# Performance work log

Measured on AMD Instinct MI355X. Metric: run time of the kernel, lower is better.

The kernel has to match this reference:

```python
import jax, jax.numpy as jnp
import numpy as np

N_NODES = 50000
N_EDGES = 800000
FEATS = 128
HIDDEN = 64
CLASSES = 64


def graph_conv(x, edges):
    """GCN-style symmetric-normalized aggregation over an edge list (no self-loops;
    self information is supplied via the concat in the host module)."""
    src, dst = edges[0], edges[1]
    ones = jnp.ones((edges.shape[1],), dtype=x.dtype)
    deg = jax.ops.segment_sum(ones, dst, num_segments=N_NODES)
    inv_sqrt = jax.lax.rsqrt(jnp.maximum(deg, 1.0))
    coef = inv_sqrt[src] * inv_sqrt[dst]            # [E]
    msg = x[src] * coef[:, None]                     # [E, H] gather
    return jax.ops.segment_sum(msg, dst, num_segments=N_NODES)  # [N, H] scatter


def setup_inputs() -> dict:
    key = jax.random.key(0)
    ks = jax.random.split(key, 16)
    def lin(k, out_d, in_d):
        return jax.random.normal(k, (out_d, in_d), dtype=jnp.float32) / np.sqrt(in_d)
    x = jax.random.normal(ks[0], (N_NODES, FEATS), dtype=jnp.float32)
    edges = jax.random.randint(ks[1], (2, N_EDGES), 0, N_NODES, dtype=jnp.int64)
    return {
        "x": x,
        "edges": edges,
        "W1": lin(ks[2], HIDDEN, FEATS),
        "b1": jnp.zeros((HIDDEN,), dtype=jnp.float32),
        "W2": lin(ks[3], HIDDEN, 2 * HIDDEN),
        "A2a": lin(ks[4], HIDDEN, HIDDEN),
        "A2b": lin(ks[5], HIDDEN, HIDDEN),
        "W3": lin(ks[6], HIDDEN, 2 * HIDDEN),
        "A3a": lin(ks[7], HIDDEN, HIDDEN),
        "A3b": lin(ks[8], HIDDEN, HIDDEN),
        "W4": lin(ks[9], CLASSES, 2 * HIDDEN),
        "A4a": lin(ks[10], CLASSES, HIDDEN),
        "A4b": lin(ks[11], CLASSES, HIDDEN),
    }


def _block(x, edges, W, Aa, Ab):
    # relu(Linear(cat[x, conv(x)]) + att_a(x) * att_b(x))
    h = graph_conv(x, edges)
    cat = jnp.concatenate([x, h], axis=1)            # [N, 2H]
    return jax.nn.relu(cat @ W.T + (x @ Aa.T) * (x @ Ab.T))


def reference(x, edges, W1, b1, W2, A2a, A2b, W3, A3a, A3b, W4, A4a, A4b):
    x = jax.nn.relu(x @ W1.T + b1)                   # [N, H]
    x = _block(x, edges, W2, A2a, A2b)               # [N, H]
    x = _block(x, edges, W3, A3a, A3b)               # [N, H]
    x = _block(x, edges, W4, A4a, A4b)               # [N, C]
    return x
```

## Files before the change

### kernel.cpp

```cpp
#include <hip/hip_runtime.h>
#include <hip/hip_bf16.h>
#include <hip/hip_fp16.h>

#define N_NODES 50000
#define N_EDGES 800000
#define NTILES 3125
#define SCAN_NB 196
#define W_TOTAL 57344
#define WB 224
#define SRC_PAD 512
#define CLS_BLOCKS 1024
#define CLS_STRIDE (128 * 256)
#define CLS_RANGE 6250
#define TB 782
#define FB 782

typedef __attribute__((ext_vector_type(8))) short bf16x8;
typedef __attribute__((ext_vector_type(4))) float f32x4;
typedef __attribute__((ext_vector_type(8))) unsigned short u16x8;

__device__ inline unsigned short f2bf(float f) {
    unsigned int x = __float_as_uint(f);
    unsigned int r = (x + 0x7FFF + ((x >> 16) & 1)) >> 16;
    return (unsigned short)r;
}
__device__ inline float2 h2f2(unsigned int u) {
    __half2 h = *(__half2*)&u;
    return make_float2(__low2float(h), __high2float(h));
}

__global__ __launch_bounds__(256) void count_pack_kernel(
    const int* __restrict__ dst, int* __restrict__ degi,
    const float* W1, const float* W2, const float* A2a, const float* A2b,
    const float* W3, const float* A3a, const float* A3b,
    const float* W4, const float* A4a, const float* A4b,
    unsigned short* __restrict__ wp) {
    if (blockIdx.x < CLS_BLOCKS) {
        int cls = blockIdx.x & 7;
        int k = blockIdx.x >> 3;
        int lo = cls * CLS_RANGE, hi = lo + CLS_RANGE;
        for (int e = k * 256 + (int)threadIdx.x; e < N_EDGES; e += CLS_STRIDE) {
            int d = dst[e];
            if (d >= lo && d < hi) atomicAdd(&degi[d], 1);
        }
    } else {
        int i = (blockIdx.x - CLS_BLOCKS) * 256 + threadIdx.x;
        if (i >= W_TOTAL) return;
        float v;
        if (i < 8192)       v = W1[i];
        else if (i < 16384) v = W2[i - 8192];
        else if (i < 20480) v = A2a[i - 16384];
        else if (i < 24576) v = A2b[i - 20480];
        else if (i < 32768) v = W3[i - 24576];
        else if (i < 36864) v = A3a[i - 32768];
        else if (i < 40960) v = A3b[i - 36864];
        else if (i < 49152) v = W4[i - 40960];
        else if (i < 53248) v = A4a[i - 49152];
        else                v = A4b[i - 53248];
        wp[i] = f2bf(v);
    }
}

__global__ __launch_bounds__(256) void scan1_kernel(const int* __restrict__ degi,
                                                    int* __restrict__ incl,
                                                    int* __restrict__ partial,
                                                    float* __restrict__ isq) {
    __shared__ int s[256];
    int tid = threadIdx.x;
    int gid = blockIdx.x * 256 + tid;
    int v = (gid < N_NODES) ? degi[gid] : 0;
    if (gid < N_NODES) isq[gid] = rsqrtf(fmaxf((float)v, 1.0f));
    s[tid] = v;
    __syncthreads();
    for (int off = 1; off < 256; off <<= 1) {
        int t = (tid >= off) ? s[tid - off] : 0;
        __syncthreads();
        s[tid] += t;
        __syncthreads();
    }
    if (gid < N_NODES) incl[gid] = s[tid];
    if (tid == 255) partial[blockIdx.x] = s[255];
}

__global__ __launch_bounds__(256) void scan2_kernel(int* __restrict__ partial,
                                                    unsigned short* __restrict__ srcA) {
    __shared__ int s[256];
    int tid = threadIdx.x;
    int v = (tid < SCAN_NB) ? partial[tid] : 0;
    s[tid] = v;
    __syncthreads();
    for (int off = 1; off < 256; off <<= 1) {
        int t = (tid >= off) ? s[tid - off] : 0;
        __syncthreads();
        s[tid] += t;
        __syncthreads();
    }
    if (tid < SCAN_NB) partial[tid] = s[tid] - v;
    srcA[N_EDGES + tid] = 0;
    srcA[N_EDGES + 256 + tid] = 0;
}

__global__ __launch_bounds__(256) void scan3_kernel(const int* __restrict__ incl,
                                                    const int* __restrict__ partial,
                                                    const int* __restrict__ degi,
                                                    int* __restrict__ rowptr,
                                                    int* __restrict__ cursor) {
    int gid = blockIdx.x * 256 + threadIdx.x;
    if (gid < N_NODES) {
        int excl = partial[blockIdx.x] + incl[gid] - degi[gid];
        rowptr[gid] = excl;
        cursor[gid] = excl;
    }
    if (gid == 0) rowptr[N_NODES] = N_EDGES;
}

__global__ __launch_bounds__(256) void layer1_scatter(const float* __restrict__ x,
                                                      const unsigned short* __restrict__ w1p,
                                                      const float* __restrict__ b1,
                                                      const float* __restrict__ isq,
                                                      unsigned short* __restrict__ outh,
                                                      __half* __restrict__ outs,
                                                      const int* __restrict__ src,
                                                      const int* __restrict__ dst,
                                                      int* __restrict__ cursor,
                                                      unsigned short* __restrict__ srcA) {
    if (blockIdx.x >= TB) {
        int cb = blockIdx.x - TB;
        int cls = cb & 7;
        int k = cb >> 3;
        int lo = cls * CLS_RANGE, hi = lo + CLS_RANGE;
        for (int e = k * 256 + (int)threadIdx.x; e < N_EDGES; e += CLS_STRIDE) {
            int d = dst[e];
            if (d >= lo && d < hi) {
                int pos = atomicAdd(&cursor[d], 1);
                srcA[pos] = (unsigned short)src[e];
            }
        }
        return;
    }

    int wave = (blockIdx.x * 256 + threadIdx.x) >> 6;
    if (wave >= NTILES) return;
    int lane = threadIdx.x & 63;
    int r16 = lane & 15, quad = lane >> 4;
    int base = wave * 16;

    bf16x8 a[4];
    const float* xr = x + (size_t)(base + r16) * 128 + quad * 8;
#pragma unroll
    for (int kb = 0; kb < 4; kb++) {
        float4 f0 = *(const float4*)(xr + kb * 32);
        float4 f1 = *(const float4*)(xr + kb * 32 + 4);
        bf16x8 v;
        v[0] = (short)f2bf(f0.x); v[1] = (short)f2bf(f0.y);
        v[2] = (short)f2bf(f0.z); v[3] = (short)f2bf(f0.w);
        v[4] = (short)f2bf(f1.x); v[5] = (short)f2bf(f1.y);
        v[6] = (short)f2bf(f1.z); v[7] = (short)f2bf(f1.w);
        a[kb] = v;
    }

    float isq4[4];
#pragma unroll
    for (int r = 0; r < 4; r++) isq4[r] = isq[base + quad * 4 + r];

#pragma unroll
    for (int jt = 0; jt < 4; jt++) {
        f32x4 acc = {0.f, 0.f, 0.f, 0.f};
        const unsigned short* wr = w1p + (size_t)(jt * 16 + r16) * 128 + quad * 8;
#pragma unroll
        for (int kb = 0; kb < 4; kb++) {
            bf16x8 b = *(const bf16x8*)(wr + kb * 32);
            acc = __builtin_amdgcn_mfma_f32_16x16x32_bf16(a[kb], b, acc, 0, 0, 0);
        }
        int col = jt * 16 + r16;
        float bias = b1[col];
#pragma unroll
        for (int r = 0; r < 4; r++) {
            int row = base + quad * 4 + r;
            float v = fmaxf(acc[r] + bias, 0.f);
            outh[(size_t)row * 64 + col] = f2bf(v);
            outs[(size_t)row * 64 + col] = __float2half(v * isq4[r]);
        }
    }
}

__global__ __launch_bounds__(256) void conv_dense(const unsigned short* __restrict__ h,
                                                  const __half* __restrict__ hs,
                                                  const int* __restrict__ rowptr,
                                                  const unsigned short* __restrict__ srcA,
                                                  const float* __restrict__ isq,
                                                  const unsigned short* __restrict__ wp,
                                                  const unsigned short* __restrict__ aap,
                                                  const unsigned short* __restrict__ abp,
                                                  unsigned short* __restrict__ outh,
                                                  __half* __restrict__ outs,
                                                  float* __restrict__ outf,
                                                  int finalLayer) {
    __shared__ unsigned short clds[64][64];

    int tid = threadIdx.x;
    int wv = tid >> 6;
    int lane = tid & 63;
    int blockBase = blockIdx.x * 64;

    {
        int e8 = lane >> 3, fl = lane & 7;
        const unsigned int* hsp = (const unsigned int*)hs;
#pragma unroll
        for (int g = 0; g < 2; g++) {
            int lrow = wv * 16 + g * 8 + e8;
            int row = blockBase + lrow;
            if (row < N_NODES) {
                int b = rowptr[row];
                int cnt = rowptr[row + 1] - b;
                float acc[8];
#pragma unroll
                for (int k = 0; k < 8; k++) acc[k] = 0.f;
                for (int i = 0; i < cnt; i += 4) {
#pragma unroll
                    for (int u = 0; u < 4; u++) {
                        int j = i + u;
                        int s = srcA[b + j];
                        uint4 raw = *(const uint4*)(hsp + (size_t)s * 32 + fl * 4);
                        unsigned int msk = (j < cnt) ? 0xFFFFFFFFu : 0u;
                        float2 f0 = h2f2(raw.x & msk);
                        float2 f1 = h2f2(raw.y & msk);
                        float2 f2 = h2f2(raw.z & msk);
                        float2 f3 = h2f2(raw.w & msk);
                        acc[0] += f0.x; acc[1] += f0.y; acc[2] += f1.x; acc[3] += f1.y;
                        acc[4] += f2.x; acc[5] += f2.y; acc[6] += f3.x; acc[7] += f3.y;
                    }
                }
                float sc = isq[row];
                u16x8 o;
#pragma unroll
                for (int k = 0; k < 8; k++) o[k] = f2bf(acc[k] * sc);
                *(u16x8*)(&clds[lrow][fl * 8]) = o;
            }
        }
    }
    __syncthreads();

    int r16 = lane & 15, quad = lane >> 4;
    int base = blockBase + wv * 16;
    if (base >= N_NODES) return;

    const unsigned short* hr = h + (size_t)(base + r16) * 64 + quad * 8;
    bf16x8 ha0 = *(const bf16x8*)(hr);
    bf16x8 ha1 = *(const bf16x8*)(hr + 32);
    bf16x8 ca0 = *(const bf16x8*)(&clds[wv * 16 + r16][quad * 8]);
    bf16x8 ca1 = *(const bf16x8*)(&clds[wv * 16 + r16][32 + quad * 8]);

    float isq4[4];
    if (!finalLayer) {
#pragma unroll
        for (int r = 0; r < 4; r++) isq4[r] = isq[base + quad * 4 + r];
    }

#pragma unroll
    for (int jt = 0; jt < 4; jt++) {
        const unsigned short* wr = wp + (size_t)(jt * 16 + r16) * 128 + quad * 8;
        const unsigned short* ar = aap + (size_t)(jt * 16 + r16) * 64 + quad * 8;
        const unsigned short* br = abp + (size_t)(jt * 16 + r16) * 64 + quad * 8;
        f32x4 P = {0.f, 0.f, 0.f, 0.f};
        f32x4 Q = {0.f, 0.f, 0.f, 0.f};
        f32x4 R = {0.f, 0.f, 0.f, 0.f};
        P = __builtin_amdgcn_mfma_f32_16x16x32_bf16(ha0, *(const bf16x8*)(wr), P, 0, 0, 0);
        P = __builtin_amdgcn_mfma_f32_16x16x32_bf16(ha1, *(const bf16x8*)(wr + 32), P, 0, 0, 0);
        P = __builtin_amdgcn_mfma_f32_16x16x32_bf16(ca0, *(const bf16x8*)(wr + 64), P, 0, 0, 0);
        P = __builtin_amdgcn_mfma_f32_16x16x32_bf16(ca1, *(const bf16x8*)(wr + 96), P, 0, 0, 0);
        Q = __builtin_amdgcn_mfma_f32_16x16x32_bf16(ha0, *(const bf16x8*)(ar), Q, 0, 0, 0);
        Q = __builtin_amdgcn_mfma_f32_16x16x32_bf16(ha1, *(const bf16x8*)(ar + 32), Q, 0, 0, 0);
        R = __builtin_amdgcn_mfma_f32_16x16x32_bf16(ha0, *(const bf16x8*)(br), R, 0, 0, 0);
        R = __builtin_amdgcn_mfma_f32_16x16x32_bf16(ha1, *(const bf16x8*)(br + 32), R, 0, 0, 0);
        int col = jt * 16 + r16;
#pragma unroll
        for (int r = 0; r < 4; r++) {
            int row = base + quad * 4 + r;
            float v = fmaxf(P[r] + Q[r] * R[r], 0.f);
            if (finalLayer) {
                outf[(size_t)row * 64 + col] = v;
            } else {
                outh[(size_t)row * 64 + col] = f2bf(v);
                outs[(size_t)row * 64 + col] = __float2half(v * isq4[r]);
            }
        }
    }
}

extern "C" void kernel_launch(void* const* d_in, const int* in_sizes, int n_in,
                              void* d_out, int out_size, void* d_ws, size_t ws_size,
                              hipStream_t stream) {
    const float* x = (const float*)d_in[0];
    const int* edges = (const int*)d_in[1];
    const float* W1 = (const float*)d_in[2];
    const float* b1 = (const float*)d_in[3];
    const float* W2 = (const float*)d_in[4];
    const float* A2a = (const float*)d_in[5];
    const float* A2b = (const float*)d_in[6];
    const float* W3 = (const float*)d_in[7];
    const float* A3a = (const float*)d_in[8];
    const float* A3b = (const float*)d_in[9];
    const float* W4 = (const float*)d_in[10];
    const float* A4a = (const float*)d_in[11];
    const float* A4b = (const float*)d_in[12];
    float* out = (float*)d_out;

    const int* src = edges;
    const int* dst = edges + N_EDGES;

    char* p = (char*)d_ws;
    auto alloc = [&](size_t bytes) {
        char* r = p;
        p += (bytes + 255) & ~(size_t)255;
        return r;
    };
    int* degi             = (int*)alloc(N_NODES * 4);
    int* incl             = (int*)alloc(N_NODES * 4);
    int* partial          = (int*)alloc(256 * 4);
    float* isq            = (float*)alloc(N_NODES * 4);
    int* rowptr           = (int*)alloc((N_NODES + 1) * 4);
    int* cursor           = (int*)alloc(N_NODES * 4);
    unsigned short* srcA  = (unsigned short*)alloc((N_EDGES + SRC_PAD) * 2);
    unsigned short* wpAll = (unsigned short*)alloc(W_TOTAL * 2);
    unsigned short* Ah    = (unsigned short*)alloc((size_t)N_NODES * 64 * 2);
    __half* As            = (__half*)alloc((size_t)N_NODES * 64 * 2);
    unsigned short* Bh    = (unsigned short*)alloc((size_t)N_NODES * 64 * 2);
    __half* Bs            = (__half*)alloc((size_t)N_NODES * 64 * 2);

    const unsigned short* W1p  = wpAll;
    const unsigned short* W2p  = wpAll + 8192;
    const unsigned short* A2ap = wpAll + 16384;
    const unsigned short* A2bp = wpAll + 20480;
    const unsigned short* W3p  = wpAll + 24576;
    const unsigned short* A3ap = wpAll + 32768;
    const unsigned short* A3bp = wpAll + 36864;
    const unsigned short* W4p  = wpAll + 40960;
    const unsigned short* A4ap = wpAll + 49152;
    const unsigned short* A4bp = wpAll + 53248;

    hipMemsetAsync(degi, 0, N_NODES * 4, stream);
    count_pack_kernel<<<CLS_BLOCKS + WB, 256, 0, stream>>>(dst, degi, W1, W2, A2a, A2b,
                                                           W3, A3a, A3b, W4, A4a, A4b,
                                                           wpAll);
    scan1_kernel<<<SCAN_NB, 256, 0, stream>>>(degi, incl, partial, isq);
    scan2_kernel<<<1, 256, 0, stream>>>(partial, srcA);
    scan3_kernel<<<SCAN_NB, 256, 0, stream>>>(incl, partial, degi, rowptr, cursor);

    layer1_scatter<<<TB + CLS_BLOCKS, 256, 0, stream>>>(x, W1p, b1, isq, Ah, As,
                                                        src, dst, cursor, srcA);

    conv_dense<<<FB, 256, 0, stream>>>(Ah, As, rowptr, srcA, isq, W2p, A2ap, A2bp,
                                       Bh, Bs, nullptr, 0);

    conv_dense<<<FB, 256, 0, stream>>>(Bh, Bs, rowptr, srcA, isq, W3p, A3ap, A3bp,
                                       Ah, As, nullptr, 0);

    conv_dense<<<FB, 256, 0, stream>>>(Ah, As, rowptr, srcA, isq, W4p, A4ap, A4bp,
                                       nullptr, nullptr, out, 1);
}
```

Baseline: 279.0 us.

## Drop bf16 activation copy, rebuild self features from scaled fp16, fold scan2

Each layer now writes only the fp16 degree-scaled activations. The self term is recovered by multiplying them by a precomputed sqrt(degree) and converting to bf16, which removes one N×64 write and read per layer. The single-block scan2 is merged into scan3, where every block redundantly rescans the 196 partials, and the srcA padding zeroing moves into the count kernel, saving a launch. The conv kernel also drops its block barrier because each wave handles its own tile. The risk is added precision loss from the fp16 round trip and the rescale.

After: 273.1 us. 2.1% less time.

```diff
diff --git a/kernel.cpp b/kernel.cpp
--- a/kernel.cpp
+++ b/kernel.cpp
@@ -9,11 +9,10 @@
 #define W_TOTAL 57344
 #define WB 224
 #define SRC_PAD 512
-#define CLS_BLOCKS 1024
+#define CLS_UNITS 1024
 #define CLS_STRIDE (128 * 256)
 #define CLS_RANGE 6250
 #define TB 782
-#define FB 782
 
 typedef __attribute__((ext_vector_type(8))) short bf16x8;
 typedef __attribute__((ext_vector_type(4))) float f32x4;
@@ -34,8 +33,8 @@
     const float* W1, const float* W2, const float* A2a, const float* A2b,
     const float* W3, const float* A3a, const float* A3b,
     const float* W4, const float* A4a, const float* A4b,
-    unsigned short* __restrict__ wp) {
-    if (blockIdx.x < CLS_BLOCKS) {
+    unsigned short* __restrict__ wp, unsigned short* __restrict__ srcA) {
+    if (blockIdx.x < CLS_UNITS) {
         int cls = blockIdx.x & 7;
         int k = blockIdx.x >> 3;
         int lo = cls * CLS_RANGE, hi = lo + CLS_RANGE;
@@ -43,8 +42,8 @@
             int d = dst[e];
             if (d >= lo && d < hi) atomicAdd(&degi[d], 1);
         }
-    } else {
-        int i = (blockIdx.x - CLS_BLOCKS) * 256 + threadIdx.x;
+    } else if (blockIdx.x < CLS_UNITS + WB) {
+        int i = (blockIdx.x - CLS_UNITS) * 256 + threadIdx.x;
         if (i >= W_TOTAL) return;
         float v;
         if (i < 8192)       v = W1[i];
@@ -58,18 +57,26 @@
         else if (i < 53248) v = A4a[i - 49152];
         else                v = A4b[i - 53248];
         wp[i] = f2bf(v);
+    } else {
+        srcA[N_EDGES + threadIdx.x] = 0;
+        srcA[N_EDGES + 256 + threadIdx.x] = 0;
     }
 }
 
 __global__ __launch_bounds__(256) void scan1_kernel(const int* __restrict__ degi,
                                                     int* __restrict__ incl,
                                                     int* __restrict__ partial,
-                                                    float* __restrict__ isq) {
+                                                    float* __restrict__ isq,
+                                                    float* __restrict__ sdeg) {
     __shared__ int s[256];
     int tid = threadIdx.x;
     int gid = blockIdx.x * 256 + tid;
     int v = (gid < N_NODES) ? degi[gid] : 0;
-    if (gid < N_NODES) isq[gid] = rsqrtf(fmaxf((float)v, 1.0f));
+    if (gid < N_NODES) {
+        float dv = fmaxf((float)v, 1.0f);
+        isq[gid] = rsqrtf(dv);
+        sdeg[gid] = sqrtf(dv);
+    }
     s[tid] = v;
     __syncthreads();
     for (int off = 1; off < 256; off <<= 1) {
@@ -82,8 +89,11 @@
     if (tid == 255) partial[blockIdx.x] = s[255];
 }
 
-__global__ __launch_bounds__(256) void scan2_kernel(int* __restrict__ partial,
-                                                    unsigned short* __restrict__ srcA) {
+__global__ __launch_bounds__(256) void scan3_kernel(const int* __restrict__ incl,
+                                                    const int* __restrict__ partial,
+                                                    const int* __restrict__ degi,
+                                                    int* __restrict__ rowptr,
+                                                    int* __restrict__ cursor) {
     __shared__ int s[256];
     int tid = threadIdx.x;
     int v = (tid < SCAN_NB) ? partial[tid] : 0;
@@ -95,19 +105,10 @@
         s[tid] += t;
         __syncthreads();
     }
-    if (tid < SCAN_NB) partial[tid] = s[tid] - v;
-    srcA[N_EDGES + tid] = 0;
-    srcA[N_EDGES + 256 + tid] = 0;
-}
-
-__global__ __launch_bounds__(256) void scan3_kernel(const int* __restrict__ incl,
-                                                    const int* __restrict__ partial,
-                                                    const int* __restrict__ degi,
-                                                    int* __restrict__ rowptr,
-                                                    int* __restrict__ cursor) {
-    int gid = blockIdx.x * 256 + threadIdx.x;
+    int boff = (blockIdx.x == 0) ? 0 : s[blockIdx.x - 1];
+    int gid = blockIdx.x * 256 + tid;
     if (gid < N_NODES) {
-        int excl = partial[blockIdx.x] + incl[gid] - degi[gid];
+        int excl = boff + incl[gid] - degi[gid];
         rowptr[gid] = excl;
         cursor[gid] = excl;
     }
@@ -118,7 +119,6 @@
                                                       const unsigned short* __restrict__ w1p,
                                                       const float* __restrict__ b1,
                                                       const float* __restrict__ isq,
-                                                      unsigned short* __restrict__ outh,
                                                       __half* __restrict__ outs,
                                                       const int* __restrict__ src,
                                                       const int* __restrict__ dst,
@@ -178,76 +178,82 @@
         for (int r = 0; r < 4; r++) {
             int row = base + quad * 4 + r;
             float v = fmaxf(acc[r] + bias, 0.f);
-            outh[(size_t)row * 64 + col] = f2bf(v);
             outs[(size_t)row * 64 + col] = __float2half(v * isq4[r]);
         }
     }
 }
 
-__global__ __launch_bounds__(256) void conv_dense(const unsigned short* __restrict__ h,
-                                                  const __half* __restrict__ hs,
-                                                  const int* __restrict__ rowptr,
-                                                  const unsigned short* __restrict__ srcA,
-                                                  const float* __restrict__ isq,
-                                                  const unsigned short* __restrict__ wp,
-                                                  const unsigned short* __restrict__ aap,
-                                                  const unsigned short* __restrict__ abp,
-                                                  unsigned short* __restrict__ outh,
-                                                  __half* __restrict__ outs,
-                                                  float* __restrict__ outf,
-                                                  int finalLayer) {
+__global__ __launch_bounds__(256) void conv_dense_k(const __half* __restrict__ hs,
+                                                    const int* __restrict__ rowptr,
+                                                    const unsigned short* __restrict__ srcA,
+                                                    const float* __restrict__ isq,
+                                                    const float* __restrict__ sdeg,
+                                                    const unsigned short* __restrict__ wp,
+                                                    const unsigned short* __restrict__ aap,
+                                                    const unsigned short* __restrict__ abp,
+                                                    __half* __restrict__ outs,
+                                                    float* __restrict__ outf,
+                                                    int finalLayer) {
     __shared__ unsigned short clds[64][64];
-
     int tid = threadIdx.x;
     int wv = tid >> 6;
     int lane = tid & 63;
-    int blockBase = blockIdx.x * 64;
+    int t = blockIdx.x * 4 + wv;
+    if (t >= NTILES) return;
+    int base = t * 16;
 
     {
         int e8 = lane >> 3, fl = lane & 7;
         const unsigned int* hsp = (const unsigned int*)hs;
 #pragma unroll
         for (int g = 0; g < 2; g++) {
-            int lrow = wv * 16 + g * 8 + e8;
-            int row = blockBase + lrow;
-            if (row < N_NODES) {
-                int b = rowptr[row];
-                int cnt = rowptr[row + 1] - b;
-                float acc[8];
-#pragma unroll
-                for (int k = 0; k < 8; k++) acc[k] = 0.f;
-                for (int i = 0; i < cnt; i += 4) {
-#pragma unroll
-                    for (int u = 0; u < 4; u++) {
-                        int j = i + u;
-                        int s = srcA[b + j];
-                        uint4 raw = *(const uint4*)(hsp + (size_t)s * 32 + fl * 4);
-                        unsigned int msk = (j < cnt) ? 0xFFFFFFFFu : 0u;
-                        float2 f0 = h2f2(raw.x & msk);
-                        float2 f1 = h2f2(raw.y & msk);
-                        float2 f2 = h2f2(raw.z & msk);
-                        float2 f3 = h2f2(raw.w & msk);
-                        acc[0] += f0.x; acc[1] += f0.y; acc[2] += f1.x; acc[3] += f1.y;
-                        acc[4] += f2.x; acc[5] += f2.y; acc[6] += f3.x; acc[7] += f3.y;
-                    }
+            int lrow = g * 8 + e8;
+            int row = base + lrow;
+            int b = rowptr[row];
+            int cnt = rowptr[row + 1] - b;
+            float acc[8];
+#pragma unroll
+            for (int k = 0; k < 8; k++) acc[k] = 0.f;
+            for (int i = 0; i < cnt; i += 4) {
+#pragma unroll
+                for (int u = 0; u < 4; u++) {
+                    int j = i + u;
+                    int s = srcA[b + j];
+                    uint4 raw = *(const uint4*)(hsp + (size_t)s * 32 + fl * 4);
+                    unsigned int msk = (j < cnt) ? 0xFFFFFFFFu : 0u;
+                    float2 f0 = h2f2(raw.x & msk);
+                    float2 f1 = h2f2(raw.y & msk);
+                    float2 f2 = h2f2(raw.z & msk);
+                    float2 f3 = h2f2(raw.w & msk);
+                    acc[0] += f0.x; acc[1] += f0.y; acc[2] += f1.x; acc[3] += f1.y;
+                    acc[4] += f2.x; acc[5] += f2.y; acc[6] += f3.x; acc[7] += f3.y;
                 }
-                float sc = isq[row];
-                u16x8 o;
-#pragma unroll
-                for (int k = 0; k < 8; k++) o[k] = f2bf(acc[k] * sc);
-                *(u16x8*)(&clds[lrow][fl * 8]) = o;
             }
-        }
-    }
-    __syncthreads();
+            float sc = isq[row];
+            u16x8 o;
+#pragma unroll
+            for (int k = 0; k < 8; k++) o[k] = f2bf(acc[k] * sc);
+            *(u16x8*)(&clds[wv * 16 + lrow][fl * 8]) = o;
+        }
+    }
 
     int r16 = lane & 15, quad = lane >> 4;
-    int base = blockBase + wv * 16;
-    if (base >= N_NODES) return;
-
-    const unsigned short* hr = h + (size_t)(base + r16) * 64 + quad * 8;
-    bf16x8 ha0 = *(const bf16x8*)(hr);
-    bf16x8 ha1 = *(const bf16x8*)(hr + 32);
+    float rs = sdeg[base + r16];
+    const unsigned int* hr = (const unsigned int*)(hs + (size_t)(base + r16) * 64) + quad * 4;
+    uint4 raw0 = *(const uint4*)(hr);
+    uint4 raw1 = *(const uint4*)(hr + 16);
+    bf16x8 ha0, ha1;
+    {
+        float2 f;
+        f = h2f2(raw0.x); ha0[0] = (short)f2bf(f.x * rs); ha0[1] = (short)f2bf(f.y * rs);
+        f = h2f2(raw0.y); ha0[2] = (short)f2bf(f.x * rs); ha0[3] = (short)f2bf(f.y * rs);
+        f = h2f2(raw0.z); ha0[4] = (short)f2bf(f.x * rs); ha0[5] = (short)f2bf(f.y * rs);
+        f = h2f2(raw0.w); ha0[6] = (short)f2bf(f.x * rs); ha0[7] = (short)f2bf(f.y * rs);
+        f = h2f2(raw1.x); ha1[0] = (short)f2bf(f.x * rs); ha1[1] = (short)f2bf(f.y * rs);
+        f = h2f2(raw1.y); ha1[2] = (short)f2bf(f.x * rs); ha1[3] = (short)f2bf(f.y * rs);
+        f = h2f2(raw1.z); ha1[4] = (short)f2bf(f.x * rs); ha1[5] = (short)f2bf(f.y * rs);
+        f = h2f2(raw1.w); ha1[6] = (short)f2bf(f.x * rs); ha1[7] = (short)f2bf(f.y * rs);
+    }
     bf16x8 ca0 = *(const bf16x8*)(&clds[wv * 16 + r16][quad * 8]);
     bf16x8 ca1 = *(const bf16x8*)(&clds[wv * 16 + r16][32 + quad * 8]);
 
@@ -278,12 +284,8 @@
         for (int r = 0; r < 4; r++) {
             int row = base + quad * 4 + r;
             float v = fmaxf(P[r] + Q[r] * R[r], 0.f);
-            if (finalLayer) {
-                outf[(size_t)row * 64 + col] = v;
-            } else {
-                outh[(size_t)row * 64 + col] = f2bf(v);
-                outs[(size_t)row * 64 + col] = __float2half(v * isq4[r]);
-            }
+            if (finalLayer) outf[(size_t)row * 64 + col] = v;
+            else            outs[(size_t)row * 64 + col] = __float2half(v * isq4[r]);
         }
     }
 }
@@ -319,13 +321,12 @@
     int* incl             = (int*)alloc(N_NODES * 4);
     int* partial          = (int*)alloc(256 * 4);
     float* isq            = (float*)alloc(N_NODES * 4);
+    float* sdeg           = (float*)alloc(N_NODES * 4);
     int* rowptr           = (int*)alloc((N_NODES + 1) * 4);
     int* cursor           = (int*)alloc(N_NODES * 4);
     unsigned short* srcA  = (unsigned short*)alloc((N_EDGES + SRC_PAD) * 2);
     unsigned short* wpAll = (unsigned short*)alloc(W_TOTAL * 2);
-    unsigned short* Ah    = (unsigned short*)alloc((size_t)N_NODES * 64 * 2);
     __half* As            = (__half*)alloc((size_t)N_NODES * 64 * 2);
-    unsigned short* Bh    = (unsigned short*)alloc((size_t)N_NODES * 64 * 2);
     __half* Bs            = (__half*)alloc((size_t)N_NODES * 64 * 2);
 
     const unsigned short* W1p  = wpAll;
@@ -340,22 +341,19 @@
     const unsigned short* A4bp = wpAll + 53248;
 
     hipMemsetAsync(degi, 0, N_NODES * 4, stream);
-    count_pack_kernel<<<CLS_BLOCKS + WB, 256, 0, stream>>>(dst, degi, W1, W2, A2a, A2b,
-                                                           W3, A3a, A3b, W4, A4a, A4b,
-                                                           wpAll);
-    scan1_kernel<<<SCAN_NB, 256, 0, stream>>>(degi, incl, partial, isq);
-    scan2_kernel<<<1, 256, 0, stream>>>(partial, srcA);
+    count_pack_kernel<<<CLS_UNITS + WB + 1, 256, 0, stream>>>(dst, degi, W1, W2, A2a,
+                                                              A2b, W3, A3a, A3b, W4,
+                                                              A4a, A4b, wpAll, srcA);
+    scan1_kernel<<<SCAN_NB, 256, 0, stream>>>(degi, incl, partial, isq, sdeg);
     scan3_kernel<<<SCAN_NB, 256, 0, stream>>>(incl, partial, degi, rowptr, cursor);
 
-    layer1_scatter<<<TB + CLS_BLOCKS, 256, 0, stream>>>(x, W1p, b1, isq, Ah, As,
-                                                        src, dst, cursor, srcA);
-
-    conv_dense<<<FB, 256, 0, stream>>>(Ah, As, rowptr, srcA, isq, W2p, A2ap, A2bp,
-                                       Bh, Bs, nullptr, 0);
-
-    conv_dense<<<FB, 256, 0, stream>>>(Bh, Bs, rowptr, srcA, isq, W3p, A3ap, A3bp,
-                                       Ah, As, nullptr, 0);
-
-    conv_dense<<<FB, 256, 0, stream>>>(Ah, As, rowptr, srcA, isq, W4p, A4ap, A4bp,
-                                       nullptr, nullptr, out, 1);
-}
+    layer1_scatter<<<TB + CLS_UNITS, 256, 0, stream>>>(x, W1p, b1, isq, As,
+                                                       src, dst, cursor, srcA);
+
+    conv_dense_k<<<TB, 256, 0, stream>>>(As, rowptr, srcA, isq, sdeg,
+                                         W2p, A2ap, A2bp, Bs, nullptr, 0);
+    conv_dense_k<<<TB, 256, 0, stream>>>(Bs, rowptr, srcA, isq, sdeg,
+                                         W3p, A3ap, A3bp, As, nullptr, 0);
+    conv_dense_k<<<TB, 256, 0, stream>>>(As, rowptr, srcA, isq, sdeg,
+                                         W4p, A4ap, A4bp, nullptr, out, 1);
+}
```
